# Performance work log

Measured on AMD Instinct MI355X. Metric: run time of the kernel, lower is better.

## Reference

```python
import jax, jax.numpy as jnp
import numpy as np

SIGMA = 8.0          # self.sigama
IGNORE_THR = 0.5     # self.ignore_threshold

def _clog(p):
    # torch BCELoss clamps log at -100
    return jnp.clip(jnp.log(jnp.clip(p, 1e-12, 1.0)), -100.0, 0.0)

def _bce(p, t):
    return -(t * _clog(p) + (1.0 - t) * _clog(1.0 - p))

def _smooth_l1(a, b):
    d = jnp.abs(a - b)
    return jnp.where(d < 1.0, 0.5 * d * d, d - 0.5)

def setup_inputs() -> dict:
    key = jax.random.key(0)
    k1, k2, k3, k4, k5 = jax.random.split(key, 5)
    bs, T, C, H, W = 32, 50, 80, 76, 76
    inp = jax.random.normal(k1, (bs, 5 + C, H, W), dtype=jnp.float32) * 0.5
    cls = jax.random.randint(k2, (bs, T, 1), 0, C).astype(jnp.float32)
    xy = jax.random.uniform(k3, (bs, T, 2), minval=0.02, maxval=0.98)
    wh = jax.random.uniform(k4, (bs, T, 2), minval=0.02, maxval=0.30)
    targets = jnp.concatenate([cls, xy, wh], -1)
    # variable number of valid targets per image; zero rows are skipped by the loss
    nvalid = jax.random.randint(k5, (bs,), 5, T)
    tmask = (jnp.arange(T)[None, :] < nvalid[:, None]).astype(jnp.float32)
    targets = targets * tmask[..., None]
    return {"input": inp, "targets": targets}

def reference(input, targets):
    bs, A, H, W = input.shape
    C = A - 5
    T = targets.shape[1]
    dt = input.dtype

    pred = jnp.transpose(input, (0, 2, 3, 1))  # [bs,H,W,A]
    x = jax.nn.sigmoid(pred[..., 0])
    y = jax.nn.sigmoid(pred[..., 1])
    w = pred[..., 2]
    h = pred[..., 3]
    conf = jax.nn.sigmoid(pred[..., 4])
    pred_cls = jax.nn.sigmoid(pred[..., 5:])

    gx_grid = jnp.arange(W, dtype=dt)[None, None, :]
    gy_grid = jnp.arange(H, dtype=dt)[None, :, None]
    pred_boxes = jnp.stack([x + gx_grid, y + gy_grid,
                            jnp.exp(w) * SIGMA, jnp.exp(h) * SIGMA], -1)
    pb = jax.lax.stop_gradient(pred_boxes)  # .detach() in original

    # ---- vectorized get_target ----
    valid = jnp.sum(targets, -1) != 0                      # [bs,T]
    gx = targets[..., 1] * W
    gy = targets[..., 2] * H
    gw = targets[..., 3] * W
    gh = targets[..., 4] * H
    gi = jnp.clip(gx.astype(jnp.int32), 0, W - 1)
    gj = jnp.clip(gy.astype(jnp.int32), 0, H - 1)
    cells = gj * W + gi
    # duplicate-cell skip: a target is dropped if an earlier VALID target hit the same cell
    tri = jnp.tril(jnp.ones((T, T), bool), -1)             # [t, t'] true iff t' < t
    dup = jnp.any((cells[:, :, None] == cells[:, None, :]) & valid[:, None, :] & tri[None], -1)
    eff = valid & ~dup
    efff = eff.astype(dt)
    n_obj = jnp.sum(efff)

    # IoU of every effective gt box vs all grid pred boxes (center format)
    g = jnp.stack([gx, gy, gw, gh], -1)[:, :, None, :]      # [bs,T,1,4]
    p = pb.reshape(bs, 1, H * W, 4)                         # [bs,1,HW,4]
    gx1, gy1 = g[..., 0] - g[..., 2] / 2, g[..., 1] - g[..., 3] / 2
    gx2, gy2 = g[..., 0] + g[..., 2] / 2, g[..., 1] + g[..., 3] / 2
    px1, py1 = p[..., 0] - p[..., 2] / 2, p[..., 1] - p[..., 3] / 2
    px2, py2 = p[..., 0] + p[..., 2] / 2, p[..., 1] + p[..., 3] / 2
    iw = jnp.clip(jnp.minimum(gx2, px2) - jnp.maximum(gx1, px1), 0.0)
    ih = jnp.clip(jnp.minimum(gy2, py2) - jnp.maximum(gy1, py1), 0.0)
    inter = iw * ih
    iou = inter / (g[..., 2] * g[..., 3] + p[..., 2] * p[..., 3] - inter + 1e-16)
    iou = iou.reshape(bs, T, H, W)
    ignore = jnp.any((iou >= IGNORE_THR) & eff[:, :, None, None], 1)  # [bs,H,W]

    bidx = jnp.broadcast_to(jnp.arange(bs)[:, None], (bs, T))
    def scat(vals):
        return jnp.zeros((bs, H, W), dt).at[bidx, gj, gi].add(efff * vals)
    mask = scat(jnp.ones_like(efff))
    scales = scat(2.0 - targets[..., 3] * targets[..., 4])
    tx = scat(gx - gi.astype(dt))
    ty = scat(gy - gj.astype(dt))
    tw = scat(jnp.log(gw / SIGMA + 1e-16))
    th = scat(jnp.log(gh / SIGMA + 1e-16))
    cls_idx = jnp.clip(targets[..., 0].astype(jnp.int32), 0, C - 1)
    tcls = jnp.zeros((bs, H, W, C), dt).at[bidx, gj, gi, cls_idx].add(efff)
    noobj_mask = jnp.where(ignore | (mask > 0), 0.0, 1.0).astype(dt)

    # ---- losses (all lambdas are 1) ----
    loss_x = (mask * scales * _bce(x, tx)).sum() / n_obj
    loss_y = (mask * scales * _bce(y, ty)).sum() / n_obj
    loss_w = (mask * scales * _smooth_l1(w, tw)).sum() / n_obj
    loss_h = (mask * scales * _smooth_l1(h, th)).sum() / n_obj
    loss_conf = (_bce(conf * mask, mask).sum()
                 + 0.5 * _bce(noobj_mask * conf, jnp.zeros_like(conf)).sum()) / n_obj
    loss_tcls = jnp.where(jnp.sum(tcls) > 0,
                          (mask[..., None] * _bce(pred_cls, tcls)).sum() / n_obj,
                          jnp.zeros((), dt))
    loss = loss_x + loss_y + loss_w + loss_h + loss_conf + loss_tcls
    return (loss, loss_x, loss_y, loss_w, loss_h, loss_conf, loss_tcls)
```

## Files before the change

kernel.cpp:

```cpp
#include <hip/hip_runtime.h>
#include <math.h>

#define BS 32
#define NT 50
#define NC 80
#define H 76
#define W 76
#define HW (H*W)
#define NA (5+NC)
#define SIGMA 8.0f
#define YBLK 23
#define NBLK (BS*YBLK)

__device__ __forceinline__ float clog_(float p){
    p = fminf(fmaxf(p, 1e-12f), 1.0f);
    float l = logf(p);
    return fminf(fmaxf(l, -100.0f), 0.0f);
}

__device__ __forceinline__ float sigmoid_(float v){
    return 1.0f / (1.0f + expf(-v));
}

__global__ __launch_bounds__(64) void prep_k(
    const float* __restrict__ targets,
    float4*      __restrict__ tdata,
    int*         __restrict__ counts)
{
    const int b = blockIdx.x;
    const int t = threadIdx.x;
    __shared__ int s_cell[NT];
    __shared__ unsigned char s_valid[NT];
    __shared__ int s_count;
    if (t == 0) s_count = 0;

    float cls=0.f, xx=0.f, yy=0.f, ww=0.f, hh=0.f;
    bool valid = false;
    int cell0 = 0;
    if (t < NT){
        const float* p = targets + ((size_t)b*NT + t)*5;
        cls = p[0]; xx = p[1]; yy = p[2]; ww = p[3]; hh = p[4];
        valid = ((cls + xx + yy + ww + hh) != 0.0f);
        float gx = xx * (float)W, gy = yy * (float)H;
        int gi = min(max((int)gx, 0), W-1);
        int gj = min(max((int)gy, 0), H-1);
        cell0 = gj*W + gi;
        s_cell[t]  = cell0;
        s_valid[t] = valid ? 1 : 0;
    }
    __syncthreads();
    if (t < NT && valid){
        bool dup = false;
        for (int u = 0; u < t; ++u)
            if (s_valid[u] && s_cell[u] == cell0) dup = true;
        if (!dup){
            int idx = atomicAdd(&s_count, 1);
            float gx = xx*(float)W, gy = yy*(float)H;
            float gw = ww*(float)W, gh = hh*(float)H;
            int gi = min(max((int)gx, 0), W-1);
            int gj = min(max((int)gy, 0), H-1);
            float4* d = tdata + ((size_t)b*NT + idx)*3;
            d[0] = make_float4(gx - gw*0.5f, gy - gh*0.5f,
                               gx + gw*0.5f, gy + gh*0.5f);
            d[1] = make_float4(gx - (float)gi, gy - (float)gj,
                               logf(gw/SIGMA + 1e-16f),
                               logf(gh/SIGMA + 1e-16f));
            d[2] = make_float4(2.0f - ww*hh,
                               (float)min(max((int)cls, 0), NC-1),
                               (float)cell0,
                               gw * gh);
        }
    }
    __syncthreads();
    if (t == 0) counts[b] = s_count;
}

__global__ __launch_bounds__(256) void yolo_main(
    const float*  __restrict__ input,
    const float4* __restrict__ tdata,
    const int*    __restrict__ counts,
    float*        __restrict__ partials)
{
    const int b   = blockIdx.x;
    const int yb  = blockIdx.y;
    const int tid = threadIdx.x;
    const int bid = b * YBLK + yb;

    __shared__ float4 s_t4[NT*3];
    __shared__ int s_nb;

    if (tid < NT*3) s_t4[tid] = tdata[(size_t)b*NT*3 + tid];
    if (tid == 0)   s_nb = counts[b];

    const int cellLo = yb * 256;
    const int cell   = cellLo + tid;
    const float* binp = input + (size_t)b*NA*HW;
    float vx=0.f, vy=0.f, vw=0.f, vh=0.f, vc=0.f;
    const bool incell = (cell < HW);
    if (incell){
        const float* base = binp + cell;
        vx = base[0];
        vy = base[HW];
        vw = base[2*HW];
        vh = base[3*HW];
        vc = base[4*HW];
    }
    __syncthreads();
    const int nb = s_nb;

    float lx=0.f, ly=0.f, lw=0.f, lh=0.f, lc=0.f, lt=0.f;

    const int cellHi = (cellLo + 256 < HW) ? cellLo + 256 : HW;
    for (int t = 0; t < nb; ++t){
        float4 meta = s_t4[3*t+2];
        int q = (int)meta.z;
        if (q >= cellLo && q < cellHi && tid < NC){
            float pc = sigmoid_(binp[(size_t)(5+tid)*HW + q]);
            int cidx = (int)meta.y;
            lt += (tid == cidx) ? -clog_(pc) : -clog_(1.f - pc);
        }
    }

    if (incell){
        float x    = sigmoid_(vx);
        float y    = sigmoid_(vy);
        float conf = sigmoid_(vc);
        int i = cell / W, j = cell - i*W;
        float pw = expf(vw) * SIGMA;
        float ph = expf(vh) * SIGMA;
        float px = x + (float)j;
        float py = y + (float)i;
        float px1 = px - pw*0.5f, px2 = px + pw*0.5f;
        float py1 = py - ph*0.5f, py2 = py + ph*0.5f;
        float parea = pw * ph;

        bool ignore = false;
        int myt = -1;
        for (int t = 0; t < nb; ++t){
            float4 bx   = s_t4[3*t];
            float4 meta = s_t4[3*t+2];
            float iw = fminf(bx.z, px2) - fmaxf(bx.x, px1);
            float ih = fminf(bx.w, py2) - fmaxf(bx.y, py1);
            iw = fmaxf(iw, 0.f); ih = fmaxf(ih, 0.f);
            float inter = iw * ih;
            ignore = ignore || (inter >= 0.5f*(meta.w + parea - inter + 1e-16f));
            if ((int)meta.z == cell) myt = t;
        }

        if (myt >= 0){
            float4 r    = s_t4[3*myt+1];
            float scale = s_t4[3*myt+2].x;
            lx = scale * (-(r.x*clog_(x) + (1.f-r.x)*clog_(1.f-x)));
            ly = scale * (-(r.y*clog_(y) + (1.f-r.y)*clog_(1.f-y)));
            float dw = fabsf(vw - r.z);
            lw = scale * (dw < 1.f ? 0.5f*dw*dw : dw - 0.5f);
            float dh = fabsf(vh - r.w);
            lh = scale * (dh < 1.f ? 0.5f*dh*dh : dh - 0.5f);
            lc = -clog_(conf);
        } else if (!ignore){
            lc = 0.5f * (-clog_(1.0f - conf));
        }
    }

    #pragma unroll
    for (int off = 32; off > 0; off >>= 1){
        lx += __shfl_down(lx, off);
        ly += __shfl_down(ly, off);
        lw += __shfl_down(lw, off);
        lh += __shfl_down(lh, off);
        lc += __shfl_down(lc, off);
        lt += __shfl_down(lt, off);
    }
    __shared__ float s_red[4*6];
    if ((tid & 63) == 0){
        int wv = tid >> 6;
        s_red[wv*6+0] = lx; s_red[wv*6+1] = ly; s_red[wv*6+2] = lw;
        s_red[wv*6+3] = lh; s_red[wv*6+4] = lc; s_red[wv*6+5] = lt;
    }
    __syncthreads();
    if (tid < 6){
        float v = s_red[tid] + s_red[6+tid] + s_red[12+tid] + s_red[18+tid];
        partials[tid*NBLK + bid] = v;
    }
}

__global__ __launch_bounds__(256) void finalize_k(
    const float* __restrict__ partials,
    const int*   __restrict__ counts,
    float*       __restrict__ out)
{
    int tid = threadIdx.x;
    float loc[6] = {0,0,0,0,0,0};
    for (int k = tid; k < NBLK; k += 256){
        #pragma unroll
        for (int j = 0; j < 6; ++j) loc[j] += partials[j*NBLK + k];
    }
    float nloc = (tid < BS) ? (float)counts[tid] : 0.f;

    #pragma unroll
    for (int off = 32; off > 0; off >>= 1){
        #pragma unroll
        for (int j = 0; j < 6; ++j) loc[j] += __shfl_down(loc[j], off);
        nloc += __shfl_down(nloc, off);
    }
    __shared__ float s_red[4*7];
    if ((tid & 63) == 0){
        int wv = tid >> 6;
        #pragma unroll
        for (int j = 0; j < 6; ++j) s_red[wv*7+j] = loc[j];
        s_red[wv*7+6] = nloc;
    }
    __syncthreads();
    if (tid == 0){
        float s[7];
        #pragma unroll
        for (int j = 0; j < 7; ++j)
            s[j] = s_red[j] + s_red[7+j] + s_red[14+j] + s_red[21+j];
        float n = s[6];
        float inv = (n > 0.f) ? (1.0f / n) : 0.0f;
        float lx = s[0]*inv, ly = s[1]*inv, lw = s[2]*inv, lh = s[3]*inv;
        float lconf = s[4]*inv;
        float ltcls = (n > 0.f) ? s[5]*inv : 0.0f;
        out[0] = lx + ly + lw + lh + lconf + ltcls;
        out[1] = lx;
        out[2] = ly;
        out[3] = lw;
        out[4] = lh;
        out[5] = lconf;
        out[6] = ltcls;
    }
}

extern "C" void kernel_launch(void* const* d_in, const int* in_sizes, int n_in,
                              void* d_out, int out_size, void* d_ws, size_t ws_size,
                              hipStream_t stream) {
    const float* input   = (const float*)d_in[0];
    const float* targets = (const float*)d_in[1];
    float* out = (float*)d_out;

    float4* tdata    = (float4*)d_ws;
    float*  partials = (float*)((char*)d_ws + 76800);
    int*    counts   = (int*)((char*)d_ws + 76800 + 6*NBLK*sizeof(float));

    prep_k<<<dim3(BS), dim3(64), 0, stream>>>(targets, tdata, counts);

    dim3 grid(BS, YBLK);
    yolo_main<<<grid, dim3(256), 0, stream>>>(input, tdata, counts, partials);

    finalize_k<<<1, dim3(256), 0, stream>>>(partials, counts, out);
}
```

Measured before the change: 109.0 us.

## Process three cells per thread and use fast sigmoid/log intrinsics

Each block now covers HW/8 cells, and each thread handles up to three cells. One pass over the target list serves all three cells, so the shared-memory target reads in the IoU/ignore loop are amortized and the class-loss gather loop runs over fewer blocks. The block count falls from 736 to 256, which lets finalize_k read exactly one partial per thread with no loop. Sigmoid and log switch to fast intrinsics (__expf, __logf, rcp), which trades some precision for fewer instructions, and the smaller grid lowers parallelism across the GPU.

```diff
diff --git a/kernel.cpp b/kernel.cpp
--- a/kernel.cpp
+++ b/kernel.cpp
@@ -9,17 +9,18 @@
 #define HW (H*W)
 #define NA (5+NC)
 #define SIGMA 8.0f
-#define YBLK 23
-#define NBLK (BS*YBLK)
+#define NYB 8
+#define CPB (HW/NYB)
+#define NBLK (BS*NYB)
 
 __device__ __forceinline__ float clog_(float p){
     p = fminf(fmaxf(p, 1e-12f), 1.0f);
-    float l = logf(p);
+    float l = __logf(p);
     return fminf(fmaxf(l, -100.0f), 0.0f);
 }
 
 __device__ __forceinline__ float sigmoid_(float v){
-    return 1.0f / (1.0f + expf(-v));
+    return __builtin_amdgcn_rcpf(1.0f + __expf(-v));
 }
 
 __global__ __launch_bounds__(64) void prep_k(
@@ -75,6 +76,26 @@
     if (t == 0) counts[b] = s_count;
 }
 
+struct Acc { float lx, ly, lw, lh, lc; };
+__device__ __forceinline__ void cell_loss(
+    Acc& a, const float4* s_t4, int myt, bool ignore,
+    float x, float y, float vw, float vh, float conf)
+{
+    if (myt >= 0){
+        float4 r    = s_t4[3*myt+1];
+        float scale = s_t4[3*myt+2].x;
+        a.lx += scale * (-(r.x*clog_(x) + (1.f-r.x)*clog_(1.f-x)));
+        a.ly += scale * (-(r.y*clog_(y) + (1.f-r.y)*clog_(1.f-y)));
+        float dw = fabsf(vw - r.z);
+        a.lw += scale * (dw < 1.f ? 0.5f*dw*dw : dw - 0.5f);
+        float dh = fabsf(vh - r.w);
+        a.lh += scale * (dh < 1.f ? 0.5f*dh*dh : dh - 0.5f);
+        a.lc += -clog_(conf);
+    } else if (!ignore){
+        a.lc += 0.5f * (-clog_(1.0f - conf));
+    }
+}
+
 __global__ __launch_bounds__(256) void yolo_main(
     const float*  __restrict__ input,
     const float4* __restrict__ tdata,
@@ -84,84 +105,101 @@
     const int b   = blockIdx.x;
     const int yb  = blockIdx.y;
     const int tid = threadIdx.x;
-    const int bid = b * YBLK + yb;
+    const int bid = b * NYB + yb;
 
     __shared__ float4 s_t4[NT*3];
     __shared__ int s_nb;
-
     if (tid < NT*3) s_t4[tid] = tdata[(size_t)b*NT*3 + tid];
     if (tid == 0)   s_nb = counts[b];
 
-    const int cellLo = yb * 256;
-    const int cell   = cellLo + tid;
+    const int blockLo = yb * CPB;
+    const int blockHi = blockLo + CPB;
     const float* binp = input + (size_t)b*NA*HW;
-    float vx=0.f, vy=0.f, vw=0.f, vh=0.f, vc=0.f;
-    const bool incell = (cell < HW);
-    if (incell){
-        const float* base = binp + cell;
-        vx = base[0];
-        vy = base[HW];
-        vw = base[2*HW];
-        vh = base[3*HW];
-        vc = base[4*HW];
-    }
+
+    const int  cell0 = blockLo + tid;
+    const int  cell1 = cell0 + 256;
+    const bool in2   = (tid < CPB - 512);
+    const int  cell2 = in2 ? (cell0 + 512) : cell0;
+
+    float vx0=binp[cell0], vy0=binp[HW+cell0], vw0=binp[2*HW+cell0],
+          vh0=binp[3*HW+cell0], vc0=binp[4*HW+cell0];
+    float vx1=binp[cell1], vy1=binp[HW+cell1], vw1=binp[2*HW+cell1],
+          vh1=binp[3*HW+cell1], vc1=binp[4*HW+cell1];
+    float vx2=binp[cell2], vy2=binp[HW+cell2], vw2=binp[2*HW+cell2],
+          vh2=binp[3*HW+cell2], vc2=binp[4*HW+cell2];
+
     __syncthreads();
     const int nb = s_nb;
 
-    float lx=0.f, ly=0.f, lw=0.f, lh=0.f, lc=0.f, lt=0.f;
-
-    const int cellHi = (cellLo + 256 < HW) ? cellLo + 256 : HW;
+    float lt = 0.f;
+    if (tid < NC){
+        for (int t = 0; t < nb; ++t){
+            float4 meta = s_t4[3*t+2];
+            int q = (int)meta.z;
+            if (q >= blockLo && q < blockHi){
+                float pc  = sigmoid_(binp[(size_t)(5+tid)*HW + q]);
+                float arg = (tid == (int)meta.y) ? pc : 1.f - pc;
+                lt += -clog_(arg);
+            }
+        }
+    }
+
+    float x0 = sigmoid_(vx0), y0 = sigmoid_(vy0), cf0 = sigmoid_(vc0);
+    float x1 = sigmoid_(vx1), y1 = sigmoid_(vy1), cf1 = sigmoid_(vc1);
+    float x2 = sigmoid_(vx2), y2 = sigmoid_(vy2), cf2 = sigmoid_(vc2);
+    float pw0 = __expf(vw0)*SIGMA, ph0 = __expf(vh0)*SIGMA;
+    float pw1 = __expf(vw1)*SIGMA, ph1 = __expf(vh1)*SIGMA;
+    float pw2 = __expf(vw2)*SIGMA, ph2 = __expf(vh2)*SIGMA;
+
+    int i0 = cell0 / W, j0 = cell0 - i0*W;
+    int i1 = cell1 / W, j1 = cell1 - i1*W;
+    int i2 = cell2 / W, j2 = cell2 - i2*W;
+
+    float px10 = x0 + j0 - pw0*0.5f, px20 = x0 + j0 + pw0*0.5f;
+    float py10 = y0 + i0 - ph0*0.5f, py20 = y0 + i0 + ph0*0.5f;
+    float pa0  = pw0 * ph0;
+    float px11 = x1 + j1 - pw1*0.5f, px21 = x1 + j1 + pw1*0.5f;
+    float py11 = y1 + i1 - ph1*0.5f, py21 = y1 + i1 + ph1*0.5f;
+    float pa1  = pw1 * ph1;
+    float px12 = x2 + j2 - pw2*0.5f, px22 = x2 + j2 + pw2*0.5f;
+    float py12 = y2 + i2 - ph2*0.5f, py22 = y2 + i2 + ph2*0.5f;
+    float pa2  = pw2 * ph2;
+
+    bool ig0=false, ig1=false, ig2=false;
+    int  myt0=-1,  myt1=-1,  myt2=-1;
     for (int t = 0; t < nb; ++t){
+        float4 bx   = s_t4[3*t];
         float4 meta = s_t4[3*t+2];
-        int q = (int)meta.z;
-        if (q >= cellLo && q < cellHi && tid < NC){
-            float pc = sigmoid_(binp[(size_t)(5+tid)*HW + q]);
-            int cidx = (int)meta.y;
-            lt += (tid == cidx) ? -clog_(pc) : -clog_(1.f - pc);
-        }
-    }
-
-    if (incell){
-        float x    = sigmoid_(vx);
-        float y    = sigmoid_(vy);
-        float conf = sigmoid_(vc);
-        int i = cell / W, j = cell - i*W;
-        float pw = expf(vw) * SIGMA;
-        float ph = expf(vh) * SIGMA;
-        float px = x + (float)j;
-        float py = y + (float)i;
-        float px1 = px - pw*0.5f, px2 = px + pw*0.5f;
-        float py1 = py - ph*0.5f, py2 = py + ph*0.5f;
-        float parea = pw * ph;
-
-        bool ignore = false;
-        int myt = -1;
-        for (int t = 0; t < nb; ++t){
-            float4 bx   = s_t4[3*t];
-            float4 meta = s_t4[3*t+2];
-            float iw = fminf(bx.z, px2) - fmaxf(bx.x, px1);
-            float ih = fminf(bx.w, py2) - fmaxf(bx.y, py1);
-            iw = fmaxf(iw, 0.f); ih = fmaxf(ih, 0.f);
-            float inter = iw * ih;
-            ignore = ignore || (inter >= 0.5f*(meta.w + parea - inter + 1e-16f));
-            if ((int)meta.z == cell) myt = t;
-        }
-
-        if (myt >= 0){
-            float4 r    = s_t4[3*myt+1];
-            float scale = s_t4[3*myt+2].x;
-            lx = scale * (-(r.x*clog_(x) + (1.f-r.x)*clog_(1.f-x)));
-            ly = scale * (-(r.y*clog_(y) + (1.f-r.y)*clog_(1.f-y)));
-            float dw = fabsf(vw - r.z);
-            lw = scale * (dw < 1.f ? 0.5f*dw*dw : dw - 0.5f);
-            float dh = fabsf(vh - r.w);
-            lh = scale * (dh < 1.f ? 0.5f*dh*dh : dh - 0.5f);
-            lc = -clog_(conf);
-        } else if (!ignore){
-            lc = 0.5f * (-clog_(1.0f - conf));
-        }
-    }
-
+        int qc = (int)meta.z;
+        {
+            float iw = fminf(bx.z, px20) - fmaxf(bx.x, px10);
+            float ih = fminf(bx.w, py20) - fmaxf(bx.y, py10);
+            float inter = fmaxf(iw,0.f)*fmaxf(ih,0.f);
+            ig0 = ig0 || (inter >= 0.5f*(meta.w + pa0 - inter + 1e-16f));
+            if (qc == cell0) myt0 = t;
+        }
+        {
+            float iw = fminf(bx.z, px21) - fmaxf(bx.x, px11);
+            float ih = fminf(bx.w, py21) - fmaxf(bx.y, py11);
+            float inter = fmaxf(iw,0.f)*fmaxf(ih,0.f);
+            ig1 = ig1 || (inter >= 0.5f*(meta.w + pa1 - inter + 1e-16f));
+            if (qc == cell1) myt1 = t;
+        }
+        {
+            float iw = fminf(bx.z, px22) - fmaxf(bx.x, px12);
+            float ih = fminf(bx.w, py22) - fmaxf(bx.y, py12);
+            float inter = fmaxf(iw,0.f)*fmaxf(ih,0.f);
+            ig2 = ig2 || (inter >= 0.5f*(meta.w + pa2 - inter + 1e-16f));
+            if (in2 && qc == cell2) myt2 = t;
+        }
+    }
+
+    Acc a = {0.f,0.f,0.f,0.f,0.f};
+    cell_loss(a, s_t4, myt0, ig0, x0, y0, vw0, vh0, cf0);
+    cell_loss(a, s_t4, myt1, ig1, x1, y1, vw1, vh1, cf1);
+    if (in2) cell_loss(a, s_t4, myt2, ig2, x2, y2, vw2, vh2, cf2);
+
+    float lx=a.lx, ly=a.ly, lw=a.lw, lh=a.lh, lc=a.lc;
     #pragma unroll
     for (int off = 32; off > 0; off >>= 1){
         lx += __shfl_down(lx, off);
@@ -190,11 +228,9 @@
     float*       __restrict__ out)
 {
     int tid = threadIdx.x;
-    float loc[6] = {0,0,0,0,0,0};
-    for (int k = tid; k < NBLK; k += 256){
-        #pragma unroll
-        for (int j = 0; j < 6; ++j) loc[j] += partials[j*NBLK + k];
-    }
+    float loc[6];
+    #pragma unroll
+    for (int j = 0; j < 6; ++j) loc[j] = partials[j*NBLK + tid];
     float nloc = (tid < BS) ? (float)counts[tid] : 0.f;
 
     #pragma unroll
@@ -244,7 +280,7 @@
 
     prep_k<<<dim3(BS), dim3(64), 0, stream>>>(targets, tdata, counts);
 
-    dim3 grid(BS, YBLK);
+    dim3 grid(BS, NYB);
     yolo_main<<<grid, dim3(256), 0, stream>>>(input, tdata, counts, partials);
 
     finalize_k<<<1, dim3(256), 0, stream>>>(partials, counts, out);
```

After: 113.0 us. 1.04x slower.
